# Kernel optimization log

Hardware: AMD Instinct MI355X
Metric: run time of the kernel (lower is better)

## Reference

```python
import jax, jax.numpy as jnp
import numpy as np
from jax import lax

NUM_CLASSES = 80
BOX_GAIN, CLS_GAIN, OBJ_GAIN = 7.5, 0.5, 1.0
LABEL_SMOOTH = 0.0
BATCH, NUM_T, IMG = 16, 256, 640
EPS = 1e-7


def setup_inputs() -> dict:
    key = jax.random.key(0)
    ks = jax.random.split(key, 10)
    inp = {}
    for i, g in enumerate([80, 40, 20]):
        inp[f"cls_p{i}"] = jax.random.normal(ks[i], (BATCH, NUM_CLASSES, g, g), jnp.float32)
        inp[f"reg_p{i}"] = jax.random.normal(ks[3 + i], (BATCH, 4, g, g), jnp.float32) * 0.5
    cxy = jax.random.uniform(ks[6], (NUM_T, 2), minval=32.0, maxval=float(IMG - 32))
    wh = jax.random.uniform(ks[7], (NUM_T, 2), minval=8.0, maxval=128.0)
    inp["tboxes"] = jnp.concatenate([cxy - wh / 2, cxy + wh / 2], axis=-1)  # [T,4] xyxy px
    inp["t_batch"] = jax.random.randint(ks[8], (NUM_T,), 0, BATCH, jnp.int32)
    inp["t_cls"] = jax.random.randint(ks[9], (NUM_T,), 0, NUM_CLASSES, jnp.int32)
    return inp


def _bce(z, t):
    # BCEWithLogits: softplus(z) - z*t, numerically stable
    return jnp.logaddexp(0.0, z) - z * t


def _box_iou(a, b):
    # a: [B,A,4] xyxy, b: [T,4] xyxy -> [B,A,T]
    lt = jnp.maximum(a[:, :, None, :2], b[None, None, :, :2])
    rb = jnp.minimum(a[:, :, None, 2:], b[None, None, :, 2:])
    wh = jnp.clip(rb - lt, 0.0)
    inter = wh[..., 0] * wh[..., 1]
    area_a = (a[..., 2] - a[..., 0]) * (a[..., 3] - a[..., 1])
    area_b = (b[:, 2] - b[:, 0]) * (b[:, 3] - b[:, 1])
    return inter / (area_a[:, :, None] + area_b[None, None, :] - inter + EPS)


def _ciou(p, g):
    # elementwise CIoU between matched boxes, p/g: [B,A,4] xyxy -> [B,A]
    pw, ph = p[..., 2] - p[..., 0], p[..., 3] - p[..., 1]
    gw, gh = g[..., 2] - g[..., 0], g[..., 3] - g[..., 1]
    lt = jnp.maximum(p[..., :2], g[..., :2])
    rb = jnp.minimum(p[..., 2:], g[..., 2:])
    wh = jnp.clip(rb - lt, 0.0)
    inter = wh[..., 0] * wh[..., 1]
    union = pw * ph + gw * gh - inter + EPS
    iou = inter / union
    clt = jnp.minimum(p[..., :2], g[..., :2])
    crb = jnp.maximum(p[..., 2:], g[..., 2:])
    c = crb - clt
    c2 = c[..., 0] ** 2 + c[..., 1] ** 2 + EPS  # enclosing diag^2
    pc = (p[..., :2] + p[..., 2:]) * 0.5
    gc = (g[..., :2] + g[..., 2:]) * 0.5
    rho2 = jnp.sum((pc - gc) ** 2, axis=-1)  # center dist^2
    v = (4.0 / jnp.pi ** 2) * (jnp.arctan(gw / (gh + EPS)) - jnp.arctan(pw / (ph + EPS))) ** 2
    alpha = lax.stop_gradient(v / (v - iou + 1.0 + EPS))
    return iou - rho2 / c2 - alpha * v


def _scale_loss(cls_p, reg_p, tboxes, t_batch, t_cls, stride):
    B, C, H, W = cls_p.shape
    A = H * W
    cls_p = cls_p.reshape(B, C, A).transpose(0, 2, 1)  # [B,A,C]
    reg_p = reg_p.reshape(B, 4, A).transpose(0, 2, 1)  # [B,A,4]
    gy, gx = jnp.meshgrid(jnp.arange(H, dtype=jnp.float32), jnp.arange(W, dtype=jnp.float32), indexing="ij")
    grid = jnp.stack([gx, gy], axis=-1).reshape(A, 2)  # [A,2] (x,y), row-major over (h,w)
    # decode: xy = (sigmoid + grid)*stride, wh = exp*stride -> xyxy
    xy = (jax.nn.sigmoid(reg_p[..., :2]) + grid) * stride
    wh = jnp.exp(reg_p[..., 2:4]) * stride
    boxes = jnp.concatenate([xy - wh * 0.5, xy + wh * 0.5], axis=-1)  # [B,A,4]
    # pairwise IoU vs all targets, mask targets from other images
    iou = _box_iou(boxes, tboxes)  # [B,A,T]
    valid = t_batch[None, None, :] == jnp.arange(B, dtype=t_batch.dtype)[:, None, None]
    iou = jnp.where(valid, iou, -1.0)
    max_iou = jnp.max(iou, axis=-1)
    best = jnp.argmax(iou, axis=-1)  # [B,A]
    pos = max_iou > 0.5  # positive anchor mask
    npos = jnp.maximum(jnp.sum(pos), 1)
    # box loss: (1 - CIoU) averaged over positives
    mt_boxes = tboxes[best]  # [B,A,4] gathered matched GT
    ciou = _ciou(boxes, mt_boxes)
    box_loss = jnp.sum(jnp.where(pos, 1.0 - ciou, 0.0)) / npos
    # cls loss: BCE with (smoothed) one-hot over positive anchors
    cp, cn = 1.0 - 0.5 * LABEL_SMOOTH, 0.5 * LABEL_SMOOTH
    cls_t = jax.nn.one_hot(t_cls[best], C, dtype=cls_p.dtype) * (cp - cn) + cn
    cls_loss = jnp.sum(_bce(cls_p, cls_t) * pos[..., None]) / (npos * C)
    # obj loss: BCE of max class logit vs positivity, over all anchors
    obj_logit = jnp.max(cls_p, axis=-1)
    obj_loss = jnp.mean(_bce(obj_logit, pos.astype(cls_p.dtype)))
    return BOX_GAIN * box_loss + CLS_GAIN * cls_loss + OBJ_GAIN * obj_loss


def reference(cls_p0, cls_p1, cls_p2, reg_p0, reg_p1, reg_p2, tboxes, t_batch, t_cls):
    total = jnp.float32(0.0)
    for i, (c, r) in enumerate([(cls_p0, reg_p0), (cls_p1, reg_p1), (cls_p2, reg_p2)]):
        total = total + _scale_loss(c, r, tboxes, t_batch, t_cls, float(8 * 2 ** i))
    return total
```

## Files before the change

kernel.cpp:

```cpp
#include <hip/hip_runtime.h>
#include <math.h>

#define C_NUM 80
#define T_NUM 256
#define EPSF  1e-7f

#define PBLK_OFF 64

__device__ __forceinline__ float softplusf(float z) {
    return fmaxf(z, 0.0f) + log1pf(expf(-fabsf(z)));
}

__device__ __forceinline__ void tile_decode(int tile, int& s, int& b, int& chunk,
                                            int& H, float& stride) {
    if (tile < 400)      { s = 0; b = tile / 25;             chunk = tile % 25; H = 80; stride =  8.f; }
    else if (tile < 512) { int r = tile - 400; s = 1; b = r / 7; chunk = r % 7; H = 40; stride = 16.f; }
    else                 { int r = tile - 512; s = 2; b = r / 2; chunk = r % 2; H = 20; stride = 32.f; }
}

__global__ __launch_bounds__(256)
void yolo_fused(const float* __restrict__ cls0, const float* __restrict__ cls1,
                const float* __restrict__ cls2,
                const float* __restrict__ reg0, const float* __restrict__ reg1,
                const float* __restrict__ reg2,
                const float* __restrict__ tboxes, const int* __restrict__ t_batch,
                const int* __restrict__ t_cls,
                unsigned int* __restrict__ counter, float4* __restrict__ pblk,
                float* __restrict__ out)
{
    __shared__ float s_x1[T_NUM], s_y1[T_NUM], s_x2[T_NUM], s_y2[T_NUM], s_ar[T_NUM];
    __shared__ int   s_tc[T_NUM];
    __shared__ int   s_list[T_NUM];
    __shared__ int   s_wcnt[4];
    __shared__ float4 s_wmax[4][4][16];
    __shared__ int   s_btc[T_NUM] __attribute__((aligned(16)));
    __shared__ float s_red[4][4];
    __shared__ int   s_last;

    const int tid = threadIdx.x;
    const int bid = blockIdx.x;
    int s, b, chunk, H; float stride;
    tile_decode(bid, s, b, chunk, H, stride);
    const int A = H * H;
    const float* clsp = (s == 0) ? cls0 : (s == 1) ? cls1 : cls2;
    const float* regp = (s == 0) ? reg0 : (s == 1) ? reg1 : reg2;

    {
        float4 t4 = reinterpret_cast<const float4*>(tboxes)[tid];
        s_x1[tid] = t4.x; s_y1[tid] = t4.y; s_x2[tid] = t4.z; s_y2[tid] = t4.w;
        s_ar[tid] = (t4.z - t4.x) * (t4.w - t4.y);
        s_tc[tid] = t_cls[tid];
    }
    const int lane = tid & 63, wave = tid >> 6;
    int match = (t_batch[tid] == b) ? 1 : 0;
    unsigned long long mask = __ballot(match != 0);
    if (lane == 0) s_wcnt[wave] = __popcll(mask);
    __syncthreads();
    int base = 0;
    #pragma unroll
    for (int w = 0; w < 4; ++w) if (w < wave) base += s_wcnt[w];
    const int nT = s_wcnt[0] + s_wcnt[1] + s_wcnt[2] + s_wcnt[3];
    if (match) {
        int pfx = __popcll(mask & (((unsigned long long)1 << lane) - 1ull));
        s_list[base + pfx] = tid;
    }
    __syncthreads();

    const int cq = lane >> 4, ag = lane & 15;
    const int cbase = wave * 20 + cq * 5;
    float4 z[4][5];
    #pragma unroll
    for (int st = 0; st < 4; ++st) {
        int a0 = chunk * 256 + st * 64 + 4 * ag;
        const float* pst = clsp + ((size_t)(b * C_NUM + cbase)) * (size_t)A
                         + ((a0 < A) ? a0 : 0);
        #pragma unroll
        for (int k = 0; k < 5; ++k)
            z[st][k] = *reinterpret_cast<const float4*>(pst + (size_t)k * A);
    }

    const int a = chunk * 256 + tid;
    float cnt = 0.f, boxs = 0.f;
    if (a < A) {
        const float* rp = regp + (b * 4) * A + a;
        float rx = rp[0], ry = rp[A], rw = rp[2 * A], rh = rp[3 * A];
        float gx = (float)(a % H), gy = (float)(a / H);
        float x = (1.f / (1.f + expf(-rx)) + gx) * stride;
        float y = (1.f / (1.f + expf(-ry)) + gy) * stride;
        float w = expf(rw) * stride;
        float h = expf(rh) * stride;
        float px1 = x - 0.5f * w, py1 = y - 0.5f * h;
        float px2 = x + 0.5f * w, py2 = y + 0.5f * h;
        float pw = px2 - px1, ph = py2 - py1;
        float parea = pw * ph;

        float maxiou = -1.f; int best = 0;
        for (int j = 0; j < nT; ++j) {
            int t = s_list[j];
            float ix = fminf(px2, s_x2[t]) - fmaxf(px1, s_x1[t]);
            float iy = fminf(py2, s_y2[t]) - fmaxf(py1, s_y1[t]);
            float inter = fmaxf(ix, 0.f) * fmaxf(iy, 0.f);
            float iou = inter / (parea + s_ar[t] - inter + EPSF);
            if (iou > maxiou) { maxiou = iou; best = t; }
        }
        const bool pos = maxiou > 0.5f;
        s_btc[tid] = pos ? s_tc[best] : -1;

        if (pos) {
            cnt = 1.f;
            float gx1 = s_x1[best], gy1 = s_y1[best], gx2 = s_x2[best], gy2 = s_y2[best];
            float gw = gx2 - gx1, gh = gy2 - gy1;
            float ix = fminf(px2, gx2) - fmaxf(px1, gx1);
            float iy = fminf(py2, gy2) - fmaxf(py1, gy1);
            float inter = fmaxf(ix, 0.f) * fmaxf(iy, 0.f);
            float uni = parea + gw * gh - inter + EPSF;
            float iou = inter / uni;
            float cw = fmaxf(px2, gx2) - fminf(px1, gx1);
            float ch = fmaxf(py2, gy2) - fminf(py1, gy1);
            float c2 = cw * cw + ch * ch + EPSF;
            float dx = 0.5f * ((px1 + px2) - (gx1 + gx2));
            float dy = 0.5f * ((py1 + py2) - (gy1 + gy2));
            float rho2 = dx * dx + dy * dy;
            float dv = atanf(gw / (gh + EPSF)) - atanf(pw / (ph + EPSF));
            float v = 0.40528473456935108577f * dv * dv;
            float alpha = v / (v - iou + 1.f + EPSF);
            boxs = 1.f - (iou - rho2 / c2 - alpha * v);
        }
    } else {
        s_btc[tid] = -1;
    }

    #pragma unroll
    for (int st = 0; st < 4; ++st) {
        float4 mx;
        mx.x = fmaxf(fmaxf(fmaxf(z[st][0].x, z[st][1].x), fmaxf(z[st][2].x, z[st][3].x)), z[st][4].x);
        mx.y = fmaxf(fmaxf(fmaxf(z[st][0].y, z[st][1].y), fmaxf(z[st][2].y, z[st][3].y)), z[st][4].y);
        mx.z = fmaxf(fmaxf(fmaxf(z[st][0].z, z[st][1].z), fmaxf(z[st][2].z, z[st][3].z)), z[st][4].z);
        mx.w = fmaxf(fmaxf(fmaxf(z[st][0].w, z[st][1].w), fmaxf(z[st][2].w, z[st][3].w)), z[st][4].w);
        #pragma unroll
        for (int d = 16; d <= 32; d <<= 1) {
            mx.x = fmaxf(mx.x, __shfl_xor(mx.x, d, 64));
            mx.y = fmaxf(mx.y, __shfl_xor(mx.y, d, 64));
            mx.z = fmaxf(mx.z, __shfl_xor(mx.z, d, 64));
            mx.w = fmaxf(mx.w, __shfl_xor(mx.w, d, 64));
        }
        if (cq == 0) s_wmax[wave][st][ag] = mx;
    }
    __syncthreads();

    float clss = 0.f;
    #pragma unroll
    for (int st = 0; st < 4; ++st) {
        int a0 = chunk * 256 + st * 64 + 4 * ag;
        if (a0 < A) {
            int4 t4 = *reinterpret_cast<const int4*>(&s_btc[st * 64 + 4 * ag]);
            if ((t4.x >= 0) | (t4.y >= 0) | (t4.z >= 0) | (t4.w >= 0)) {
                #pragma unroll
                for (int k = 0; k < 5; ++k) {
                    const int cg = cbase + k;
                    if (t4.x >= 0) { clss += softplusf(z[st][k].x); if (cg == t4.x) clss -= z[st][k].x; }
                    if (t4.y >= 0) { clss += softplusf(z[st][k].y); if (cg == t4.y) clss -= z[st][k].y; }
                    if (t4.z >= 0) { clss += softplusf(z[st][k].z); if (cg == t4.z) clss -= z[st][k].z; }
                    if (t4.w >= 0) { clss += softplusf(z[st][k].w); if (cg == t4.w) clss -= z[st][k].w; }
                }
            }
        }
    }

    float objs = 0.f;
    if (a < A) {
        const int st = tid >> 6, agx = (tid & 63) >> 2, comp = tid & 3;
        float m = -INFINITY;
        #pragma unroll
        for (int w = 0; w < 4; ++w)
            m = fmaxf(m, reinterpret_cast<const float*>(&s_wmax[w][st][agx])[comp]);
        bool pos = s_btc[tid] >= 0;
        objs = softplusf(m) - (pos ? m : 0.f);
    }

    #pragma unroll
    for (int off = 32; off > 0; off >>= 1) {
        cnt  += __shfl_down(cnt,  off, 64);
        boxs += __shfl_down(boxs, off, 64);
        clss += __shfl_down(clss, off, 64);
        objs += __shfl_down(objs, off, 64);
    }
    if (lane == 0) {
        s_red[wave][0] = cnt;  s_red[wave][1] = boxs;
        s_red[wave][2] = clss; s_red[wave][3] = objs;
    }
    __syncthreads();
    if (tid == 0) {
        float4 v;
        v.x = s_red[0][0] + s_red[1][0] + s_red[2][0] + s_red[3][0];
        v.y = s_red[0][1] + s_red[1][1] + s_red[2][1] + s_red[3][1];
        v.z = s_red[0][2] + s_red[1][2] + s_red[2][2] + s_red[3][2];
        v.w = s_red[0][3] + s_red[1][3] + s_red[2][3] + s_red[3][3];
        pblk[bid] = v;
        __threadfence();
        unsigned int old = atomicAdd(counter, 1u);
        s_last = (old == 543u) ? 1 : 0;
    }
    __syncthreads();

    if (s_last) {
        __threadfence();
        if (tid < 64) {
            float np0 = 0.f, np1 = 0.f, np2 = 0.f, bx0 = 0.f, bx1 = 0.f, bx2 = 0.f;
            float cl0 = 0.f, cl1 = 0.f, cl2 = 0.f, ob0 = 0.f, ob1 = 0.f, ob2 = 0.f;
            for (int i = tid; i < 544; i += 64) {
                float4 v = pblk[i];
                if (i < 400)      { np0 += v.x; bx0 += v.y; cl0 += v.z; ob0 += v.w; }
                else if (i < 512) { np1 += v.x; bx1 += v.y; cl1 += v.z; ob1 += v.w; }
                else              { np2 += v.x; bx2 += v.y; cl2 += v.z; ob2 += v.w; }
            }
            #pragma unroll
            for (int off = 32; off > 0; off >>= 1) {
                np0 += __shfl_down(np0, off, 64); np1 += __shfl_down(np1, off, 64);
                np2 += __shfl_down(np2, off, 64); bx0 += __shfl_down(bx0, off, 64);
                bx1 += __shfl_down(bx1, off, 64); bx2 += __shfl_down(bx2, off, 64);
                cl0 += __shfl_down(cl0, off, 64); cl1 += __shfl_down(cl1, off, 64);
                cl2 += __shfl_down(cl2, off, 64); ob0 += __shfl_down(ob0, off, 64);
                ob1 += __shfl_down(ob1, off, 64); ob2 += __shfl_down(ob2, off, 64);
            }
            if (tid == 0) {
                float np[3] = { fmaxf(np0, 1.f), fmaxf(np1, 1.f), fmaxf(np2, 1.f) };
                float bx[3] = { bx0, bx1, bx2 };
                float cl[3] = { cl0, cl1, cl2 };
                float ob[3] = { ob0, ob1, ob2 };
                const float inv_anch[3] = { 1.f / (16.f * 6400.f), 1.f / (16.f * 1600.f), 1.f / (16.f * 400.f) };
                float total = 0.f;
                #pragma unroll
                for (int k = 0; k < 3; ++k)
                    total += 7.5f * bx[k] / np[k]
                           + 0.5f * cl[k] / (np[k] * (float)C_NUM)
                           + ob[k] * inv_anch[k];
                out[0] = total;
            }
        }
    }
}

extern "C" void kernel_launch(void* const* d_in, const int* in_sizes, int n_in,
                              void* d_out, int out_size, void* d_ws, size_t ws_size,
                              hipStream_t stream) {
    const float *cls[3] = {nullptr, nullptr, nullptr};
    const float *reg[3] = {nullptr, nullptr, nullptr};
    const float *tboxes = nullptr;
    const int *t_batch = nullptr, *t_cls = nullptr;
    for (int i = 0; i < n_in; ++i) {
        switch (in_sizes[i]) {
            case 16 * 80 * 6400: cls[0] = (const float*)d_in[i]; break;
            case 16 * 80 * 1600: cls[1] = (const float*)d_in[i]; break;
            case 16 * 80 * 400:  cls[2] = (const float*)d_in[i]; break;
            case 16 * 4 * 6400:  reg[0] = (const float*)d_in[i]; break;
            case 16 * 4 * 1600:  reg[1] = (const float*)d_in[i]; break;
            case 16 * 4 * 400:   reg[2] = (const float*)d_in[i]; break;
            case 256 * 4:        tboxes = (const float*)d_in[i]; break;
            case 256:
                if (!t_batch) t_batch = (const int*)d_in[i];
                else          t_cls   = (const int*)d_in[i];
                break;
            default: break;
        }
    }
    unsigned int* counter = (unsigned int*)d_ws;
    float4*       pblk    = (float4*)((char*)d_ws + PBLK_OFF);
    float*        out     = (float*)d_out;

    hipMemsetAsync(counter, 0, sizeof(unsigned int), stream);
    hipLaunchKernelGGL(yolo_fused, dim3(544), dim3(256), 0, stream,
                       cls[0], cls[1], cls[2], reg[0], reg[1], reg[2],
                       tboxes, t_batch, t_cls, counter, pblk, out);
}
```

Measured before the change: 120.3 us.

## Shrink per-block tile to 64 anchors and launch four times more blocks

```diff
diff --git a/kernel.cpp b/kernel.cpp
--- a/kernel.cpp
+++ b/kernel.cpp
@@ -4,18 +4,11 @@
 #define C_NUM 80
 #define T_NUM 256
 #define EPSF  1e-7f
-
+#define NBLK  2112
 #define PBLK_OFF 64
 
 __device__ __forceinline__ float softplusf(float z) {
     return fmaxf(z, 0.0f) + log1pf(expf(-fabsf(z)));
-}
-
-__device__ __forceinline__ void tile_decode(int tile, int& s, int& b, int& chunk,
-                                            int& H, float& stride) {
-    if (tile < 400)      { s = 0; b = tile / 25;             chunk = tile % 25; H = 80; stride =  8.f; }
-    else if (tile < 512) { int r = tile - 400; s = 1; b = r / 7; chunk = r % 7; H = 40; stride = 16.f; }
-    else                 { int r = tile - 512; s = 2; b = r / 2; chunk = r % 2; H = 20; stride = 32.f; }
 }
 
 __global__ __launch_bounds__(256)
@@ -32,18 +25,21 @@
     __shared__ int   s_tc[T_NUM];
     __shared__ int   s_list[T_NUM];
     __shared__ int   s_wcnt[4];
-    __shared__ float4 s_wmax[4][4][16];
-    __shared__ int   s_btc[T_NUM] __attribute__((aligned(16)));
+    __shared__ float4 s_wmax[4][16];
+    __shared__ int   s_btc[64] __attribute__((aligned(16)));
     __shared__ float s_red[4][4];
     __shared__ int   s_last;
 
     const int tid = threadIdx.x;
     const int bid = blockIdx.x;
-    int s, b, chunk, H; float stride;
-    tile_decode(bid, s, b, chunk, H, stride);
-    const int A = H * H;
-    const float* clsp = (s == 0) ? cls0 : (s == 1) ? cls1 : cls2;
-    const float* regp = (s == 0) ? reg0 : (s == 1) ? reg1 : reg2;
+    const int lane = tid & 63, wave = tid >> 6;
+    const int cq = lane >> 4, ag = lane & 15;
+
+    int s, b, a0, A, H; float stride;
+    const float *clsp, *regp;
+    if (bid < 1600)      { s = 0; b = bid / 100;            a0 = (bid % 100) * 64; A = 6400; H = 80; stride =  8.f; clsp = cls0; regp = reg0; }
+    else if (bid < 2000) { int r = bid - 1600; s = 1; b = r / 25; a0 = (r % 25) * 64; A = 1600; H = 40; stride = 16.f; clsp = cls1; regp = reg1; }
+    else                 { int r = bid - 2000; s = 2; b = r / 7;  a0 = (r % 7)  * 64; A = 400;  H = 20; stride = 32.f; clsp = cls2; regp = reg2; }
 
     {
         float4 t4 = reinterpret_cast<const float4*>(tboxes)[tid];
@@ -51,7 +47,6 @@
         s_ar[tid] = (t4.z - t4.x) * (t4.w - t4.y);
         s_tc[tid] = t_cls[tid];
     }
-    const int lane = tid & 63, wave = tid >> 6;
     int match = (t_batch[tid] == b) ? 1 : 0;
     unsigned long long mask = __ballot(match != 0);
     if (lane == 0) s_wcnt[wave] = __popcll(mask);
@@ -66,115 +61,111 @@
     }
     __syncthreads();
 
-    const int cq = lane >> 4, ag = lane & 15;
+    const int am = a0 + lane;
+    const bool amv = am < A;
+    float rx = 0.f, ry = 0.f, rw = 0.f, rh = 0.f;
+    {
+        const float* rp = regp + (size_t)(b * 4) * (size_t)A + (amv ? am : 0);
+        if (wave == 0) { rx = rp[0]; ry = rp[A]; rw = rp[2 * (size_t)A]; rh = rp[3 * (size_t)A]; }
+    }
+
     const int cbase = wave * 20 + cq * 5;
-    float4 z[4][5];
+    const int ga = a0 + 4 * ag;
+    const float* p = clsp + ((size_t)(b * C_NUM + cbase)) * (size_t)A + ((ga < A) ? ga : a0);
+    float4 z0 = *reinterpret_cast<const float4*>(p);
+    float4 z1 = *reinterpret_cast<const float4*>(p + (size_t)A);
+    float4 z2 = *reinterpret_cast<const float4*>(p + 2 * (size_t)A);
+    float4 z3 = *reinterpret_cast<const float4*>(p + 3 * (size_t)A);
+    float4 z4 = *reinterpret_cast<const float4*>(p + 4 * (size_t)A);
+
+    float cnt = 0.f, boxs = 0.f;
+    if (wave == 0) {
+        if (amv) {
+            float gx = (float)(am % H), gy = (float)(am / H);
+            float x = (1.f / (1.f + expf(-rx)) + gx) * stride;
+            float y = (1.f / (1.f + expf(-ry)) + gy) * stride;
+            float w = expf(rw) * stride;
+            float h = expf(rh) * stride;
+            float px1 = x - 0.5f * w, py1 = y - 0.5f * h;
+            float px2 = x + 0.5f * w, py2 = y + 0.5f * h;
+            float pw = px2 - px1, ph = py2 - py1;
+            float parea = pw * ph;
+
+            float maxiou = -1.f; int best = 0;
+            for (int j = 0; j < nT; ++j) {
+                int t = s_list[j];
+                float ix = fminf(px2, s_x2[t]) - fmaxf(px1, s_x1[t]);
+                float iy = fminf(py2, s_y2[t]) - fmaxf(py1, s_y1[t]);
+                float inter = fmaxf(ix, 0.f) * fmaxf(iy, 0.f);
+                float iou = inter / (parea + s_ar[t] - inter + EPSF);
+                if (iou > maxiou) { maxiou = iou; best = t; }
+            }
+            const bool pos = maxiou > 0.5f;
+            s_btc[lane] = pos ? s_tc[best] : -1;
+
+            if (pos) {
+                cnt = 1.f;
+                float gx1 = s_x1[best], gy1 = s_y1[best], gx2 = s_x2[best], gy2 = s_y2[best];
+                float gw = gx2 - gx1, gh = gy2 - gy1;
+                float ix = fminf(px2, gx2) - fmaxf(px1, gx1);
+                float iy = fminf(py2, gy2) - fmaxf(py1, gy1);
+                float inter = fmaxf(ix, 0.f) * fmaxf(iy, 0.f);
+                float uni = parea + gw * gh - inter + EPSF;
+                float iou = inter / uni;
+                float cw = fmaxf(px2, gx2) - fminf(px1, gx1);
+                float ch = fmaxf(py2, gy2) - fminf(py1, gy1);
+                float c2 = cw * cw + ch * ch + EPSF;
+                float dx = 0.5f * ((px1 + px2) - (gx1 + gx2));
+                float dy = 0.5f * ((py1 + py2) - (gy1 + gy2));
+                float rho2 = dx * dx + dy * dy;
+                float dv = atanf(gw / (gh + EPSF)) - atanf(pw / (ph + EPSF));
+                float v = 0.40528473456935108577f * dv * dv;
+                float alpha = v / (v - iou + 1.f + EPSF);
+                boxs = 1.f - (iou - rho2 / c2 - alpha * v);
+            }
+        } else {
+            s_btc[lane] = -1;
+        }
+    }
+
+    float4 mx;
+    mx.x = fmaxf(fmaxf(fmaxf(z0.x, z1.x), fmaxf(z2.x, z3.x)), z4.x);
+    mx.y = fmaxf(fmaxf(fmaxf(z0.y, z1.y), fmaxf(z2.y, z3.y)), z4.y);
+    mx.z = fmaxf(fmaxf(fmaxf(z0.z, z1.z), fmaxf(z2.z, z3.z)), z4.z);
+    mx.w = fmaxf(fmaxf(fmaxf(z0.w, z1.w), fmaxf(z2.w, z3.w)), z4.w);
     #pragma unroll
-    for (int st = 0; st < 4; ++st) {
-        int a0 = chunk * 256 + st * 64 + 4 * ag;
-        const float* pst = clsp + ((size_t)(b * C_NUM + cbase)) * (size_t)A
-                         + ((a0 < A) ? a0 : 0);
-        #pragma unroll
-        for (int k = 0; k < 5; ++k)
-            z[st][k] = *reinterpret_cast<const float4*>(pst + (size_t)k * A);
-    }
-
-    const int a = chunk * 256 + tid;
-    float cnt = 0.f, boxs = 0.f;
-    if (a < A) {
-        const float* rp = regp + (b * 4) * A + a;
-        float rx = rp[0], ry = rp[A], rw = rp[2 * A], rh = rp[3 * A];
-        float gx = (float)(a % H), gy = (float)(a / H);
-        float x = (1.f / (1.f + expf(-rx)) + gx) * stride;
-        float y = (1.f / (1.f + expf(-ry)) + gy) * stride;
-        float w = expf(rw) * stride;
-        float h = expf(rh) * stride;
-        float px1 = x - 0.5f * w, py1 = y - 0.5f * h;
-        float px2 = x + 0.5f * w, py2 = y + 0.5f * h;
-        float pw = px2 - px1, ph = py2 - py1;
-        float parea = pw * ph;
-
-        float maxiou = -1.f; int best = 0;
-        for (int j = 0; j < nT; ++j) {
-            int t = s_list[j];
-            float ix = fminf(px2, s_x2[t]) - fmaxf(px1, s_x1[t]);
-            float iy = fminf(py2, s_y2[t]) - fmaxf(py1, s_y1[t]);
-            float inter = fmaxf(ix, 0.f) * fmaxf(iy, 0.f);
-            float iou = inter / (parea + s_ar[t] - inter + EPSF);
-            if (iou > maxiou) { maxiou = iou; best = t; }
-        }
-        const bool pos = maxiou > 0.5f;
-        s_btc[tid] = pos ? s_tc[best] : -1;
-
-        if (pos) {
-            cnt = 1.f;
-            float gx1 = s_x1[best], gy1 = s_y1[best], gx2 = s_x2[best], gy2 = s_y2[best];
-            float gw = gx2 - gx1, gh = gy2 - gy1;
-            float ix = fminf(px2, gx2) - fmaxf(px1, gx1);
-            float iy = fminf(py2, gy2) - fmaxf(py1, gy1);
-            float inter = fmaxf(ix, 0.f) * fmaxf(iy, 0.f);
-            float uni = parea + gw * gh - inter + EPSF;
-            float iou = inter / uni;
-            float cw = fmaxf(px2, gx2) - fminf(px1, gx1);
-            float ch = fmaxf(py2, gy2) - fminf(py1, gy1);
-            float c2 = cw * cw + ch * ch + EPSF;
-            float dx = 0.5f * ((px1 + px2) - (gx1 + gx2));
-            float dy = 0.5f * ((py1 + py2) - (gy1 + gy2));
-            float rho2 = dx * dx + dy * dy;
-            float dv = atanf(gw / (gh + EPSF)) - atanf(pw / (ph + EPSF));
-            float v = 0.40528473456935108577f * dv * dv;
-            float alpha = v / (v - iou + 1.f + EPSF);
-            boxs = 1.f - (iou - rho2 / c2 - alpha * v);
-        }
-    } else {
-        s_btc[tid] = -1;
-    }
-
-    #pragma unroll
-    for (int st = 0; st < 4; ++st) {
-        float4 mx;
-        mx.x = fmaxf(fmaxf(fmaxf(z[st][0].x, z[st][1].x), fmaxf(z[st][2].x, z[st][3].x)), z[st][4].x);
-        mx.y = fmaxf(fmaxf(fmaxf(z[st][0].y, z[st][1].y), fmaxf(z[st][2].y, z[st][3].y)), z[st][4].y);
-        mx.z = fmaxf(fmaxf(fmaxf(z[st][0].z, z[st][1].z), fmaxf(z[st][2].z, z[st][3].z)), z[st][4].z);
-        mx.w = fmaxf(fmaxf(fmaxf(z[st][0].w, z[st][1].w), fmaxf(z[st][2].w, z[st][3].w)), z[st][4].w);
-        #pragma unroll
-        for (int d = 16; d <= 32; d <<= 1) {
-            mx.x = fmaxf(mx.x, __shfl_xor(mx.x, d, 64));
-            mx.y = fmaxf(mx.y, __shfl_xor(mx.y, d, 64));
-            mx.z = fmaxf(mx.z, __shfl_xor(mx.z, d, 64));
-            mx.w = fmaxf(mx.w, __shfl_xor(mx.w, d, 64));
-        }
-        if (cq == 0) s_wmax[wave][st][ag] = mx;
-    }
+    for (int d = 16; d <= 32; d <<= 1) {
+        mx.x = fmaxf(mx.x, __shfl_xor(mx.x, d, 64));
+        mx.y = fmaxf(mx.y, __shfl_xor(mx.y, d, 64));
+        mx.z = fmaxf(mx.z, __shfl_xor(mx.z, d, 64));
+        mx.w = fmaxf(mx.w, __shfl_xor(mx.w, d, 64));
+    }
+    if (cq == 0) s_wmax[wave][ag] = mx;
     __syncthreads();
 
     float clss = 0.f;
-    #pragma unroll
-    for (int st = 0; st < 4; ++st) {
-        int a0 = chunk * 256 + st * 64 + 4 * ag;
-        if (a0 < A) {
-            int4 t4 = *reinterpret_cast<const int4*>(&s_btc[st * 64 + 4 * ag]);
-            if ((t4.x >= 0) | (t4.y >= 0) | (t4.z >= 0) | (t4.w >= 0)) {
-                #pragma unroll
-                for (int k = 0; k < 5; ++k) {
-                    const int cg = cbase + k;
-                    if (t4.x >= 0) { clss += softplusf(z[st][k].x); if (cg == t4.x) clss -= z[st][k].x; }
-                    if (t4.y >= 0) { clss += softplusf(z[st][k].y); if (cg == t4.y) clss -= z[st][k].y; }
-                    if (t4.z >= 0) { clss += softplusf(z[st][k].z); if (cg == t4.z) clss -= z[st][k].z; }
-                    if (t4.w >= 0) { clss += softplusf(z[st][k].w); if (cg == t4.w) clss -= z[st][k].w; }
-                }
+    {
+        int4 t4 = *reinterpret_cast<const int4*>(&s_btc[4 * ag]);
+        if ((t4.x >= 0) | (t4.y >= 0) | (t4.z >= 0) | (t4.w >= 0)) {
+            const float4 zz[5] = { z0, z1, z2, z3, z4 };
+            #pragma unroll
+            for (int k = 0; k < 5; ++k) {
+                const int cg = cbase + k;
+                if (t4.x >= 0) { clss += softplusf(zz[k].x); if (cg == t4.x) clss -= zz[k].x; }
+                if (t4.y >= 0) { clss += softplusf(zz[k].y); if (cg == t4.y) clss -= zz[k].y; }
+                if (t4.z >= 0) { clss += softplusf(zz[k].z); if (cg == t4.z) clss -= zz[k].z; }
+                if (t4.w >= 0) { clss += softplusf(zz[k].w); if (cg == t4.w) clss -= zz[k].w; }
             }
         }
     }
 
     float objs = 0.f;
-    if (a < A) {
-        const int st = tid >> 6, agx = (tid & 63) >> 2, comp = tid & 3;
+    if (wave == 0 && amv) {
         float m = -INFINITY;
         #pragma unroll
         for (int w = 0; w < 4; ++w)
-            m = fmaxf(m, reinterpret_cast<const float*>(&s_wmax[w][st][agx])[comp]);
-        bool pos = s_btc[tid] >= 0;
+            m = fmaxf(m, reinterpret_cast<const float*>(&s_wmax[w][lane >> 2])[lane & 3]);
+        bool pos = s_btc[lane] >= 0;
         objs = softplusf(m) - (pos ? m : 0.f);
     }
 
@@ -199,7 +190,7 @@
         pblk[bid] = v;
         __threadfence();
         unsigned int old = atomicAdd(counter, 1u);
-        s_last = (old == 543u) ? 1 : 0;
+        s_last = (old == NBLK - 1) ? 1 : 0;
     }
     __syncthreads();
 
@@ -208,11 +199,11 @@
         if (tid < 64) {
             float np0 = 0.f, np1 = 0.f, np2 = 0.f, bx0 = 0.f, bx1 = 0.f, bx2 = 0.f;
             float cl0 = 0.f, cl1 = 0.f, cl2 = 0.f, ob0 = 0.f, ob1 = 0.f, ob2 = 0.f;
-            for (int i = tid; i < 544; i += 64) {
+            for (int i = tid; i < NBLK; i += 64) {
                 float4 v = pblk[i];
-                if (i < 400)      { np0 += v.x; bx0 += v.y; cl0 += v.z; ob0 += v.w; }
-                else if (i < 512) { np1 += v.x; bx1 += v.y; cl1 += v.z; ob1 += v.w; }
-                else              { np2 += v.x; bx2 += v.y; cl2 += v.z; ob2 += v.w; }
+                if (i < 1600)      { np0 += v.x; bx0 += v.y; cl0 += v.z; ob0 += v.w; }
+                else if (i < 2000) { np1 += v.x; bx1 += v.y; cl1 += v.z; ob1 += v.w; }
+                else               { np2 += v.x; bx2 += v.y; cl2 += v.z; ob2 += v.w; }
             }
             #pragma unroll
             for (int off = 32; off > 0; off >>= 1) {
@@ -269,7 +260,7 @@
     float*        out     = (float*)d_out;
 
     hipMemsetAsync(counter, 0, sizeof(unsigned int), stream);
-    hipLaunchKernelGGL(yolo_fused, dim3(544), dim3(256), 0, stream,
+    hipLaunchKernelGGL(yolo_fused, dim3(NBLK), dim3(256), 0, stream,
                        cls[0], cls[1], cls[2], reg[0], reg[1], reg[2],
                        tboxes, t_batch, t_cls, counter, pblk, out);
 }
```

New measurement: 157.8 us. +31.1%, slower.
